# Performance work log

Measured on AMD Instinct MI355X. Metric: run time of the kernel, lower is better.

## Reference

```python
import jax, jax.numpy as jnp
import numpy as np

E = 64          # num_experts
DIM = 1024      # model dim
HID = 512       # per-expert FFN hidden dim
N = 65536       # total routed tokens (1024 per expert)


def setup_inputs() -> dict:
    key = jax.random.key(0)
    k_x, k1, k2, k3 = jax.random.split(key, 4)
    x = jax.random.normal(k_x, (N, DIM), dtype=jnp.float32)
    # learned params: w1/w3 [E, HID, DIM], w2 [E, DIM, HID] (trunc_normal std 0.02 ~ normal*0.02)
    w1 = jax.random.normal(k1, (E, HID, DIM), dtype=jnp.float32) * 0.02
    w2 = jax.random.normal(k2, (E, DIM, HID), dtype=jnp.float32) * 0.02
    w3 = jax.random.normal(k3, (E, HID, DIM), dtype=jnp.float32) * 0.02
    num_tokens_per_expert = jnp.full((E,), N // E, dtype=jnp.int32)
    return {"x": x, "w1": w1, "w2": w2, "w3": w3,
            "num_tokens_per_expert": num_tokens_per_expert}


def reference(x, w1, w2, w3, num_tokens_per_expert):
    # Grouped-GEMM SwiGLU expert FFN (torch._grouped_mm path, bf16 compute).
    bf16 = jnp.bfloat16
    xb = x.astype(bf16)                                   # [N, DIM]
    g = num_tokens_per_expert                             # [E] int32 group sizes
    w1t = jnp.swapaxes(w1.astype(bf16), 1, 2)             # [E, DIM, HID]
    w3t = jnp.swapaxes(w3.astype(bf16), 1, 2)             # [E, DIM, HID]
    w2t = jnp.swapaxes(w2.astype(bf16), 1, 2)             # [E, HID, DIM]
    h = jax.nn.silu(jax.lax.ragged_dot(xb, w1t, g))       # [N, HID]
    h = h * jax.lax.ragged_dot(xb, w3t, g)                # fused gate
    out = jax.lax.ragged_dot(h, w2t, g)                   # [N, DIM]
    return out.astype(x.dtype)
```

## Files before the change

### kernel.cpp

```cpp
#include <hip/hip_runtime.h>
#include <hip/hip_bf16.h>
#include <stdint.h>

#define NE   64
#define DIM  1024
#define HID  512
#define TPE  1024

typedef __attribute__((ext_vector_type(8)))  __bf16          bf16x8;
typedef __attribute__((ext_vector_type(4)))  float           f32x4;
typedef __attribute__((ext_vector_type(8)))  unsigned short  ushort8_t;
typedef __attribute__((ext_vector_type(4)))  float           float4_t;

__device__ __forceinline__ unsigned short f2bf(float f) {
  return __builtin_bit_cast(unsigned short, static_cast<__bf16>(f));
}
__device__ __forceinline__ float bf2f(unsigned short u) {
  unsigned int x = ((unsigned int)u) << 16;
  return __builtin_bit_cast(float, x);
}
__device__ __forceinline__ ushort8_t pack8(float4_t a, float4_t b) {
  ushort8_t r;
  r[0] = f2bf(a[0]); r[1] = f2bf(a[1]); r[2] = f2bf(a[2]); r[3] = f2bf(a[3]);
  r[4] = f2bf(b[0]); r[5] = f2bf(b[1]); r[6] = f2bf(b[2]); r[7] = f2bf(b[3]);
  return r;
}
__device__ __forceinline__ bf16x8 ldsfrag(const unsigned short* p) {
  return __builtin_bit_cast(bf16x8, *reinterpret_cast<const ushort8_t*>(p));
}

#define LDK 40

__device__ __forceinline__ int xcd_swizzle(int bid, int nwg) {
  return (bid & 7) * (nwg >> 3) + (bid >> 3);
}

#define P1_NKT (DIM / 32)

__global__ __launch_bounds__(512, 2) void p1_kernel(
    const float* __restrict__ X, const float* __restrict__ W1,
    const float* __restrict__ W3, unsigned short* __restrict__ H) {
  __shared__ __align__(16) unsigned short lA [2][256 * LDK];
  __shared__ __align__(16) unsigned short lB1[2][128 * LDK];
  __shared__ __align__(16) unsigned short lB3[2][128 * LDK];

  const int tile = xcd_swizzle(blockIdx.x, NE * 4 * 4);
  const int e  = tile >> 4;
  const int tm = (tile >> 2) & 3;
  const int tn = tile & 3;
  const int t  = threadIdx.x;

  const float* gA  = X  + (size_t)(e * TPE + tm * 256) * DIM;
  const float* gB1 = W1 + ((size_t)e * HID + tn * 128) * DIM;
  const float* gB3 = W3 + ((size_t)e * HID + tn * 128) * DIM;

  const int arow = t >> 1, acol = (t & 1) * 16;
  const int brow = t >> 2, bcol = (t & 3) * 8;

  auto load_g = [&](float4_t (&ra)[4], float4_t (&rb1)[2], float4_t (&rb3)[2],
                    int kt) {
    const size_t ao = (size_t)arow * DIM + kt * 32 + acol;
#pragma unroll
    for (int i = 0; i < 4; ++i)
      ra[i] = *reinterpret_cast<const float4_t*>(gA + ao + 4 * i);
    const size_t bo = (size_t)brow * DIM + kt * 32 + bcol;
    rb1[0] = *reinterpret_cast<const float4_t*>(gB1 + bo);
    rb1[1] = *reinterpret_cast<const float4_t*>(gB1 + bo + 4);
    rb3[0] = *reinterpret_cast<const float4_t*>(gB3 + bo);
    rb3[1] = *reinterpret_cast<const float4_t*>(gB3 + bo + 4);
  };
  auto store_l = [&](int buf, float4_t (&ra)[4], float4_t (&rb1)[2],
                     float4_t (&rb3)[2]) {
    const int ai = arow * LDK + acol;
    *reinterpret_cast<ushort8_t*>(&lA[buf][ai])     = pack8(ra[0], ra[1]);
    *reinterpret_cast<ushort8_t*>(&lA[buf][ai + 8]) = pack8(ra[2], ra[3]);
    const int bi = brow * LDK + bcol;
    *reinterpret_cast<ushort8_t*>(&lB1[buf][bi]) = pack8(rb1[0], rb1[1]);
    *reinterpret_cast<ushort8_t*>(&lB3[buf][bi]) = pack8(rb3[0], rb3[1]);
  };

  const int lane = t & 63;
  const int wv   = t >> 6;
  const int wr   = wv >> 1, wc = wv & 1;
  const int fr   = lane & 15;
  const int ks   = (lane >> 4) * 8;

  f32x4 acc1[4][4], acc3[4][4];
#pragma unroll
  for (int mi = 0; mi < 4; ++mi)
#pragma unroll
    for (int ni = 0; ni < 4; ++ni)
#pragma unroll
      for (int i = 0; i < 4; ++i) { acc1[mi][ni][i] = 0.f; acc3[mi][ni][i] = 0.f; }

  auto mfma_phase = [&](int buf) {
    bf16x8 b1f[4], b3f[4];
#pragma unroll
    for (int ni = 0; ni < 4; ++ni) {
      const int bi = (wc * 64 + ni * 16 + fr) * LDK + ks;
      b1f[ni] = ldsfrag(&lB1[buf][bi]);
      b3f[ni] = ldsfrag(&lB3[buf][bi]);
    }
#pragma unroll
    for (int mi = 0; mi < 4; ++mi) {
      const bf16x8 af = ldsfrag(&lA[buf][(wr * 64 + mi * 16 + fr) * LDK + ks]);
#pragma unroll
      for (int ni = 0; ni < 4; ++ni) {
        acc1[mi][ni] = __builtin_amdgcn_mfma_f32_16x16x32_bf16(af, b1f[ni], acc1[mi][ni], 0, 0, 0);
        acc3[mi][ni] = __builtin_amdgcn_mfma_f32_16x16x32_bf16(af, b3f[ni], acc3[mi][ni], 0, 0, 0);
      }
    }
  };

  float4_t ra0[4], rb10[2], rb30[2];
  float4_t ra1[4], rb11[2], rb31[2];
  load_g(ra0, rb10, rb30, 0);
  load_g(ra1, rb11, rb31, 1);

  for (int kt = 0; kt < P1_NKT; kt += 2) {
    store_l(0, ra0, rb10, rb30);
    __syncthreads();
    if (kt + 2 < P1_NKT) load_g(ra0, rb10, rb30, kt + 2);
    mfma_phase(0);

    store_l(1, ra1, rb11, rb31);
    __syncthreads();
    if (kt + 3 < P1_NKT) load_g(ra1, rb11, rb31, kt + 3);
    mfma_phase(1);
  }

  const int tokBase = e * TPE + tm * 256 + wr * 64;
  const int hidBase = tn * 128 + wc * 64;
#pragma unroll
  for (int mi = 0; mi < 4; ++mi)
#pragma unroll
    for (int ni = 0; ni < 4; ++ni)
#pragma unroll
      for (int r = 0; r < 4; ++r) {
        const int tok = tokBase + mi * 16 + (lane >> 4) * 4 + r;
        const int hid = hidBase + ni * 16 + fr;
        const float av = bf2f(f2bf(acc1[mi][ni][r]));
        const float bv = bf2f(f2bf(acc3[mi][ni][r]));
        const float s  = av / (1.0f + __expf(-av));
        H[(size_t)tok * HID + hid] = f2bf(s * bv);
      }
}

#define P2_NKT (HID / 32)

__global__ __launch_bounds__(512, 2) void p2_kernel(
    const unsigned short* __restrict__ Hin, const float* __restrict__ W2,
    float* __restrict__ OUT) {
  __shared__ __align__(16) unsigned short lA[2][256 * LDK];
  __shared__ __align__(16) unsigned short lB[2][128 * LDK];

  const int tile = xcd_swizzle(blockIdx.x, NE * 4 * 8);
  const int e  = tile >> 5;
  const int tm = (tile >> 3) & 3;
  const int tn = tile & 7;
  const int t  = threadIdx.x;

  const unsigned short* gA = Hin + (size_t)(e * TPE + tm * 256) * HID;
  const float*          gB = W2  + ((size_t)e * DIM + tn * 128) * HID;

  const int arow = t >> 1, acol = (t & 1) * 16;
  const int brow = t >> 2, bcol = (t & 3) * 8;

  auto load_g = [&](ushort8_t (&ra)[2], float4_t (&rb)[2], int kt) {
    const size_t ao = (size_t)arow * HID + kt * 32 + acol;
    ra[0] = *reinterpret_cast<const ushort8_t*>(gA + ao);
    ra[1] = *reinterpret_cast<const ushort8_t*>(gA + ao + 8);
    const size_t bo = (size_t)brow * HID + kt * 32 + bcol;
    rb[0] = *reinterpret_cast<const float4_t*>(gB + bo);
    rb[1] = *reinterpret_cast<const float4_t*>(gB + bo + 4);
  };
  auto store_l = [&](int buf, ushort8_t (&ra)[2], float4_t (&rb)[2]) {
    const int ai = arow * LDK + acol;
    *reinterpret_cast<ushort8_t*>(&lA[buf][ai])     = ra[0];
    *reinterpret_cast<ushort8_t*>(&lA[buf][ai + 8]) = ra[1];
    *reinterpret_cast<ushort8_t*>(&lB[buf][brow * LDK + bcol]) = pack8(rb[0], rb[1]);
  };

  const int lane = t & 63;
  const int wv   = t >> 6;
  const int wr   = wv >> 1, wc = wv & 1;
  const int fr   = lane & 15;
  const int ks   = (lane >> 4) * 8;

  f32x4 acc[4][4];
#pragma unroll
  for (int mi = 0; mi < 4; ++mi)
#pragma unroll
    for (int ni = 0; ni < 4; ++ni)
#pragma unroll
      for (int i = 0; i < 4; ++i) acc[mi][ni][i] = 0.f;

  auto mfma_phase = [&](int buf) {
    bf16x8 bfr[4];
#pragma unroll
    for (int ni = 0; ni < 4; ++ni)
      bfr[ni] = ldsfrag(&lB[buf][(wc * 64 + ni * 16 + fr) * LDK + ks]);
#pragma unroll
    for (int mi = 0; mi < 4; ++mi) {
      const bf16x8 af = ldsfrag(&lA[buf][(wr * 64 + mi * 16 + fr) * LDK + ks]);
#pragma unroll
      for (int ni = 0; ni < 4; ++ni)
        acc[mi][ni] = __builtin_amdgcn_mfma_f32_16x16x32_bf16(af, bfr[ni], acc[mi][ni], 0, 0, 0);
    }
  };

  ushort8_t ra0[2], ra1[2];
  float4_t  rb0[2], rb1[2];
  load_g(ra0, rb0, 0);
  load_g(ra1, rb1, 1);

  for (int kt = 0; kt < P2_NKT; kt += 2) {
    store_l(0, ra0, rb0);
    __syncthreads();
    if (kt + 2 < P2_NKT) load_g(ra0, rb0, kt + 2);
    mfma_phase(0);

    store_l(1, ra1, rb1);
    __syncthreads();
    if (kt + 3 < P2_NKT) load_g(ra1, rb1, kt + 3);
    mfma_phase(1);
  }

  const int tokBase = e * TPE + tm * 256 + wr * 64;
  const int dBase   = tn * 128 + wc * 64;
#pragma unroll
  for (int mi = 0; mi < 4; ++mi)
#pragma unroll
    for (int ni = 0; ni < 4; ++ni)
#pragma unroll
      for (int r = 0; r < 4; ++r) {
        const int tok = tokBase + mi * 16 + (lane >> 4) * 4 + r;
        const int d   = dBase + ni * 16 + fr;
        OUT[(size_t)tok * DIM + d] = bf2f(f2bf(acc[mi][ni][r]));
      }
}

extern "C" void kernel_launch(void* const* d_in, const int* in_sizes, int n_in,
                              void* d_out, int out_size, void* d_ws, size_t ws_size,
                              hipStream_t stream) {
  (void)in_sizes; (void)n_in; (void)out_size; (void)ws_size;
  const float* X  = (const float*)d_in[0];
  const float* W1 = (const float*)d_in[1];
  const float* W2 = (const float*)d_in[2];
  const float* W3 = (const float*)d_in[3];

  unsigned short* H = (unsigned short*)d_ws;
  float* OUT = (float*)d_out;

  p1_kernel<<<dim3(NE * 4 * 4), dim3(512), 0, stream>>>(X, W1, W3, H);
  p2_kernel<<<dim3(NE * 4 * 8), dim3(512), 0, stream>>>(H, W2, OUT);
}
```

Baseline: 449.7 us.

## Shrink GEMM tiles to 256-thread blocks and drop register double-buffer prefetch

Both kernels move from 512-thread blocks with 256-row tiles to 256-thread blocks with 128-row tiles (phase 1 also halves its N tile to 64), which quadruples the phase-1 grid and doubles the phase-2 grid. The two-deep register prefetch is replaced by a single-stage prefetch in a one-step loop, and A fragments are hoisted ahead of the MFMA loop. The intent is higher occupancy (three blocks per CU), lower register pressure and more blocks to balance across CUs. In exchange, the smaller tiles lower arithmetic intensity and increase reloading of X and the weights from global memory.

```diff
diff --git a/kernel.cpp b/kernel.cpp
--- a/kernel.cpp
+++ b/kernel.cpp
@@ -37,28 +37,29 @@
 
 #define P1_NKT (DIM / 32)
 
-__global__ __launch_bounds__(512, 2) void p1_kernel(
+__global__ __launch_bounds__(256, 3) void p1_kernel(
     const float* __restrict__ X, const float* __restrict__ W1,
     const float* __restrict__ W3, unsigned short* __restrict__ H) {
-  __shared__ __align__(16) unsigned short lA [2][256 * LDK];
-  __shared__ __align__(16) unsigned short lB1[2][128 * LDK];
-  __shared__ __align__(16) unsigned short lB3[2][128 * LDK];
-
-  const int tile = xcd_swizzle(blockIdx.x, NE * 4 * 4);
-  const int e  = tile >> 4;
-  const int tm = (tile >> 2) & 3;
-  const int tn = tile & 3;
+  __shared__ __align__(16) unsigned short lA [2][128 * LDK];
+  __shared__ __align__(16) unsigned short lB1[2][ 64 * LDK];
+  __shared__ __align__(16) unsigned short lB3[2][ 64 * LDK];
+
+  const int tile = xcd_swizzle(blockIdx.x, NE * 8 * 8);
+  const int e  = tile >> 6;
+  const int tm = (tile >> 3) & 7;
+  const int tn = tile & 7;
   const int t  = threadIdx.x;
 
-  const float* gA  = X  + (size_t)(e * TPE + tm * 256) * DIM;
-  const float* gB1 = W1 + ((size_t)e * HID + tn * 128) * DIM;
-  const float* gB3 = W3 + ((size_t)e * HID + tn * 128) * DIM;
+  const float* gA  = X  + (size_t)(e * TPE + tm * 128) * DIM;
+  const float* gB1 = W1 + ((size_t)e * HID + tn * 64) * DIM;
+  const float* gB3 = W3 + ((size_t)e * HID + tn * 64) * DIM;
 
   const int arow = t >> 1, acol = (t & 1) * 16;
   const int brow = t >> 2, bcol = (t & 3) * 8;
 
-  auto load_g = [&](float4_t (&ra)[4], float4_t (&rb1)[2], float4_t (&rb3)[2],
-                    int kt) {
+  float4_t ra[4], rb1[2], rb3[2];
+
+  auto load_g = [&](int kt) {
     const size_t ao = (size_t)arow * DIM + kt * 32 + acol;
 #pragma unroll
     for (int i = 0; i < 4; ++i)
@@ -69,14 +70,12 @@
     rb3[0] = *reinterpret_cast<const float4_t*>(gB3 + bo);
     rb3[1] = *reinterpret_cast<const float4_t*>(gB3 + bo + 4);
   };
-  auto store_l = [&](int buf, float4_t (&ra)[4], float4_t (&rb1)[2],
-                     float4_t (&rb3)[2]) {
+  auto store_l = [&](int buf) {
     const int ai = arow * LDK + acol;
     *reinterpret_cast<ushort8_t*>(&lA[buf][ai])     = pack8(ra[0], ra[1]);
     *reinterpret_cast<ushort8_t*>(&lA[buf][ai + 8]) = pack8(ra[2], ra[3]);
-    const int bi = brow * LDK + bcol;
-    *reinterpret_cast<ushort8_t*>(&lB1[buf][bi]) = pack8(rb1[0], rb1[1]);
-    *reinterpret_cast<ushort8_t*>(&lB3[buf][bi]) = pack8(rb3[0], rb3[1]);
+    *reinterpret_cast<ushort8_t*>(&lB1[buf][brow * LDK + bcol]) = pack8(rb1[0], rb1[1]);
+    *reinterpret_cast<ushort8_t*>(&lB3[buf][brow * LDK + bcol]) = pack8(rb3[0], rb3[1]);
   };
 
   const int lane = t & 63;
@@ -85,56 +84,49 @@
   const int fr   = lane & 15;
   const int ks   = (lane >> 4) * 8;
 
-  f32x4 acc1[4][4], acc3[4][4];
-#pragma unroll
-  for (int mi = 0; mi < 4; ++mi)
-#pragma unroll
-    for (int ni = 0; ni < 4; ++ni)
+  f32x4 acc1[4][2], acc3[4][2];
+#pragma unroll
+  for (int mi = 0; mi < 4; ++mi)
+#pragma unroll
+    for (int ni = 0; ni < 2; ++ni)
 #pragma unroll
       for (int i = 0; i < 4; ++i) { acc1[mi][ni][i] = 0.f; acc3[mi][ni][i] = 0.f; }
 
   auto mfma_phase = [&](int buf) {
-    bf16x8 b1f[4], b3f[4];
-#pragma unroll
-    for (int ni = 0; ni < 4; ++ni) {
-      const int bi = (wc * 64 + ni * 16 + fr) * LDK + ks;
+    bf16x8 b1f[2], b3f[2], af[4];
+#pragma unroll
+    for (int ni = 0; ni < 2; ++ni) {
+      const int bi = (wc * 32 + ni * 16 + fr) * LDK + ks;
       b1f[ni] = ldsfrag(&lB1[buf][bi]);
       b3f[ni] = ldsfrag(&lB3[buf][bi]);
     }
 #pragma unroll
-    for (int mi = 0; mi < 4; ++mi) {
-      const bf16x8 af = ldsfrag(&lA[buf][(wr * 64 + mi * 16 + fr) * LDK + ks]);
-#pragma unroll
-      for (int ni = 0; ni < 4; ++ni) {
-        acc1[mi][ni] = __builtin_amdgcn_mfma_f32_16x16x32_bf16(af, b1f[ni], acc1[mi][ni], 0, 0, 0);
-        acc3[mi][ni] = __builtin_amdgcn_mfma_f32_16x16x32_bf16(af, b3f[ni], acc3[mi][ni], 0, 0, 0);
+    for (int mi = 0; mi < 4; ++mi)
+      af[mi] = ldsfrag(&lA[buf][(wr * 64 + mi * 16 + fr) * LDK + ks]);
+#pragma unroll
+    for (int mi = 0; mi < 4; ++mi)
+#pragma unroll
+      for (int ni = 0; ni < 2; ++ni) {
+        acc1[mi][ni] = __builtin_amdgcn_mfma_f32_16x16x32_bf16(af[mi], b1f[ni], acc1[mi][ni], 0, 0, 0);
+        acc3[mi][ni] = __builtin_amdgcn_mfma_f32_16x16x32_bf16(af[mi], b3f[ni], acc3[mi][ni], 0, 0, 0);
       }
-    }
-  };
-
-  float4_t ra0[4], rb10[2], rb30[2];
-  float4_t ra1[4], rb11[2], rb31[2];
-  load_g(ra0, rb10, rb30, 0);
-  load_g(ra1, rb11, rb31, 1);
-
-  for (int kt = 0; kt < P1_NKT; kt += 2) {
-    store_l(0, ra0, rb10, rb30);
+  };
+
+  load_g(0);
+  for (int kt = 0; kt < P1_NKT; ++kt) {
+    const int buf = kt & 1;
+    store_l(buf);
     __syncthreads();
-    if (kt + 2 < P1_NKT) load_g(ra0, rb10, rb30, kt + 2);
-    mfma_phase(0);
-
-    store_l(1, ra1, rb11, rb31);
-    __syncthreads();
-    if (kt + 3 < P1_NKT) load_g(ra1, rb11, rb31, kt + 3);
-    mfma_phase(1);
+    if (kt + 1 < P1_NKT) load_g(kt + 1);
+    mfma_phase(buf);
   }
 
-  const int tokBase = e * TPE + tm * 256 + wr * 64;
-  const int hidBase = tn * 128 + wc * 64;
-#pragma unroll
-  for (int mi = 0; mi < 4; ++mi)
-#pragma unroll
-    for (int ni = 0; ni < 4; ++ni)
+  const int tokBase = e * TPE + tm * 128 + wr * 64;
+  const int hidBase = tn * 64 + wc * 32;
+#pragma unroll
+  for (int mi = 0; mi < 4; ++mi)
+#pragma unroll
+    for (int ni = 0; ni < 2; ++ni)
 #pragma unroll
       for (int r = 0; r < 4; ++r) {
         const int tok = tokBase + mi * 16 + (lane >> 4) * 4 + r;
@@ -148,37 +140,41 @@
 
 #define P2_NKT (HID / 32)
 
-__global__ __launch_bounds__(512, 2) void p2_kernel(
+__global__ __launch_bounds__(256, 3) void p2_kernel(
     const unsigned short* __restrict__ Hin, const float* __restrict__ W2,
     float* __restrict__ OUT) {
-  __shared__ __align__(16) unsigned short lA[2][256 * LDK];
+  __shared__ __align__(16) unsigned short lA[2][128 * LDK];
   __shared__ __align__(16) unsigned short lB[2][128 * LDK];
 
-  const int tile = xcd_swizzle(blockIdx.x, NE * 4 * 8);
-  const int e  = tile >> 5;
-  const int tm = (tile >> 3) & 3;
+  const int tile = xcd_swizzle(blockIdx.x, NE * 8 * 8);
+  const int e  = tile >> 6;
+  const int tm = (tile >> 3) & 7;
   const int tn = tile & 7;
   const int t  = threadIdx.x;
 
-  const unsigned short* gA = Hin + (size_t)(e * TPE + tm * 256) * HID;
+  const unsigned short* gA = Hin + (size_t)(e * TPE + tm * 128) * HID;
   const float*          gB = W2  + ((size_t)e * DIM + tn * 128) * HID;
 
   const int arow = t >> 1, acol = (t & 1) * 16;
-  const int brow = t >> 2, bcol = (t & 3) * 8;
-
-  auto load_g = [&](ushort8_t (&ra)[2], float4_t (&rb)[2], int kt) {
+
+  ushort8_t ra[2];
+  float4_t  rb[4];
+
+  auto load_g = [&](int kt) {
     const size_t ao = (size_t)arow * HID + kt * 32 + acol;
     ra[0] = *reinterpret_cast<const ushort8_t*>(gA + ao);
     ra[1] = *reinterpret_cast<const ushort8_t*>(gA + ao + 8);
-    const size_t bo = (size_t)brow * HID + kt * 32 + bcol;
-    rb[0] = *reinterpret_cast<const float4_t*>(gB + bo);
-    rb[1] = *reinterpret_cast<const float4_t*>(gB + bo + 4);
-  };
-  auto store_l = [&](int buf, ushort8_t (&ra)[2], float4_t (&rb)[2]) {
+    const size_t bo = (size_t)arow * HID + kt * 32 + acol;
+#pragma unroll
+    for (int i = 0; i < 4; ++i)
+      rb[i] = *reinterpret_cast<const float4_t*>(gB + bo + 4 * i);
+  };
+  auto store_l = [&](int buf) {
     const int ai = arow * LDK + acol;
     *reinterpret_cast<ushort8_t*>(&lA[buf][ai])     = ra[0];
     *reinterpret_cast<ushort8_t*>(&lA[buf][ai + 8]) = ra[1];
-    *reinterpret_cast<ushort8_t*>(&lB[buf][brow * LDK + bcol]) = pack8(rb[0], rb[1]);
+    *reinterpret_cast<ushort8_t*>(&lB[buf][ai])     = pack8(rb[0], rb[1]);
+    *reinterpret_cast<ushort8_t*>(&lB[buf][ai + 8]) = pack8(rb[2], rb[3]);
   };
 
   const int lane = t & 63;
@@ -196,37 +192,30 @@
       for (int i = 0; i < 4; ++i) acc[mi][ni][i] = 0.f;
 
   auto mfma_phase = [&](int buf) {
-    bf16x8 bfr[4];
+    bf16x8 bfr[4], af[4];
 #pragma unroll
     for (int ni = 0; ni < 4; ++ni)
       bfr[ni] = ldsfrag(&lB[buf][(wc * 64 + ni * 16 + fr) * LDK + ks]);
 #pragma unroll
-    for (int mi = 0; mi < 4; ++mi) {
-      const bf16x8 af = ldsfrag(&lA[buf][(wr * 64 + mi * 16 + fr) * LDK + ks]);
+    for (int mi = 0; mi < 4; ++mi)
+      af[mi] = ldsfrag(&lA[buf][(wr * 64 + mi * 16 + fr) * LDK + ks]);
+#pragma unroll
+    for (int mi = 0; mi < 4; ++mi)
 #pragma unroll
       for (int ni = 0; ni < 4; ++ni)
-        acc[mi][ni] = __builtin_amdgcn_mfma_f32_16x16x32_bf16(af, bfr[ni], acc[mi][ni], 0, 0, 0);
-    }
-  };
-
-  ushort8_t ra0[2], ra1[2];
-  float4_t  rb0[2], rb1[2];
-  load_g(ra0, rb0, 0);
-  load_g(ra1, rb1, 1);
-
-  for (int kt = 0; kt < P2_NKT; kt += 2) {
-    store_l(0, ra0, rb0);
+        acc[mi][ni] = __builtin_amdgcn_mfma_f32_16x16x32_bf16(af[mi], bfr[ni], acc[mi][ni], 0, 0, 0);
+  };
+
+  load_g(0);
+  for (int kt = 0; kt < P2_NKT; ++kt) {
+    const int buf = kt & 1;
+    store_l(buf);
     __syncthreads();
-    if (kt + 2 < P2_NKT) load_g(ra0, rb0, kt + 2);
-    mfma_phase(0);
-
-    store_l(1, ra1, rb1);
-    __syncthreads();
-    if (kt + 3 < P2_NKT) load_g(ra1, rb1, kt + 3);
-    mfma_phase(1);
+    if (kt + 1 < P2_NKT) load_g(kt + 1);
+    mfma_phase(buf);
   }
 
-  const int tokBase = e * TPE + tm * 256 + wr * 64;
+  const int tokBase = e * TPE + tm * 128 + wr * 64;
   const int dBase   = tn * 128 + wc * 64;
 #pragma unroll
   for (int mi = 0; mi < 4; ++mi)
@@ -252,6 +241,6 @@
   unsigned short* H = (unsigned short*)d_ws;
   float* OUT = (float*)d_out;
 
-  p1_kernel<<<dim3(NE * 4 * 4), dim3(512), 0, stream>>>(X, W1, W3, H);
-  p2_kernel<<<dim3(NE * 4 * 8), dim3(512), 0, stream>>>(H, W2, OUT);
-}
+  p1_kernel<<<dim3(NE * 8 * 8), dim3(256), 0, stream>>>(X, W1, W3, H);
+  p2_kernel<<<dim3(NE * 8 * 8), dim3(256), 0, stream>>>(H, W2, OUT);
+}
```

New measurement: 492.7 us. 9.6% more time.
